# Optimization experiments

Hardware: AMD Instinct MI355X
Metric: run time of the kernel (lower is better)

Reference implementation:

```python
import jax, jax.numpy as jnp
import numpy as np

RS, RC = 3.0, 6.0
N_AXIS = 8
N_NODES, N_ENV, N_EDGES = 50000, 1000000, 200000
N_ATOM = 4
NEURONS = [32, 64, 64]


def setup_inputs() -> dict:
    key = jax.random.key(0)
    ks = jax.random.split(key, 10)
    env_vectors = jax.random.normal(ks[0], (N_ENV, 3), dtype=jnp.float32) * 2.0
    atom_attr = jax.random.uniform(ks[1], (N_NODES, N_ATOM), dtype=jnp.float32)
    env_index = jax.random.randint(ks[2], (2, N_ENV), 0, N_NODES)
    edge_index = jax.random.randint(ks[3], (2, N_EDGES), 0, N_NODES)
    d_in = 2 * N_ATOM + 1  # snorm + both endpoint one-hot attrs
    W1 = jax.random.normal(ks[4], (d_in, NEURONS[0]), dtype=jnp.float32) / np.sqrt(d_in)
    b1 = jnp.zeros((NEURONS[0],), jnp.float32)
    W2 = jax.random.normal(ks[5], (NEURONS[0], NEURONS[1]), dtype=jnp.float32) / np.sqrt(NEURONS[0])
    b2 = jnp.zeros((NEURONS[1],), jnp.float32)
    W3 = jax.random.normal(ks[6], (NEURONS[1], NEURONS[2]), dtype=jnp.float32) / np.sqrt(NEURONS[1])
    b3 = jnp.zeros((NEURONS[2],), jnp.float32)
    return dict(env_vectors=env_vectors, atom_attr=atom_attr, env_index=env_index,
                edge_index=edge_index, W1=W1, b1=b1, W2=W2, b2=b2, W3=W3, b3=b3)


def _smooth(r):
    # elementwise smooth cutoff: 1/r for r<rs, polynomial taper on [rs,rc), 0 beyond
    x = (r - RC) / (RS - RC)
    mid = (1.0 / r) * (x ** 3 * (10.0 + x * (-15.0 + 6.0 * x)) + 1.0)
    return jnp.where(r < RS, 1.0 / r, jnp.where(r < RC, mid, jnp.zeros_like(r)))


def reference(env_vectors, atom_attr, env_index, edge_index, W1, b1, W2, b2, W3, b3):
    n_env = env_vectors.shape[0]
    n_nodes = atom_attr.shape[0]
    r = jnp.linalg.norm(env_vectors, axis=-1, keepdims=True)          # [E,1]
    snorm = _smooth(r)
    # gather both endpoint attrs: env_index.T.flatten() interleaves (src_i, dst_i)
    env_attr = atom_attr[env_index.T.reshape(-1)].reshape(n_env, -1)  # [E, 2*n_atom]
    # ResNet embedding (residual where dims match)
    h = jnp.tanh(jnp.concatenate([snorm, env_attr], axis=-1) @ W1 + b1)
    h = jnp.tanh(h @ W2 + b2)
    h = jnp.tanh(h @ W3 + b3) + h                                     # [E, D]
    # outer product with direction vectors, scatter-mean over target node
    outer = h[:, :, None] * env_vectors[:, None, :]                   # [E, D, 3]
    idx = env_index[1]
    summ = jax.ops.segment_sum(outer, idx, num_segments=n_nodes)      # [N, D, 3]
    cnt = jax.ops.segment_sum(jnp.ones((n_env,), h.dtype), idx, num_segments=n_nodes)
    aggr = summ / jnp.clip(cnt, 1.0)[:, None, None]
    # per-node self outer-product bmm, slice first n_axis columns, flatten
    desc = jnp.einsum('nda,nea->nde', aggr, aggr)[:, :, :N_AXIS]      # [N, D, n_axis]
    node_desc = desc.reshape(n_nodes, -1)                             # [N, D*n_axis]
    edge_desc = node_desc[edge_index[0]] + node_desc[edge_index[1]]   # [Ne, D*n_axis]
    return node_desc, edge_desc
```

## Files before the change

### kernel.cpp

```cpp
#include <hip/hip_runtime.h>
#include <hip/hip_bf16.h>

#define N_NODES 50000
#define N_ENV   1000000
#define N_EDGES 200000

__device__ __forceinline__ float fast_tanh(float x){
  float xc = fminf(fmaxf(x, -10.f), 10.f);
  float t  = __expf(2.f * xc);
  return __fdividef(t - 1.f, t + 1.f);
}

__global__ void k_zero_i(int* __restrict__ p, int n){
  int i = blockIdx.x * blockDim.x + threadIdx.x;
  int stride = gridDim.x * blockDim.x;
  for (; i < n; i += stride) p[i] = 0;
}

__global__ __launch_bounds__(256) void k_hist(
    const int* __restrict__ env_index, int* __restrict__ counts)
{
  int e = blockIdx.x * 256 + threadIdx.x;
  if (e >= N_ENV) return;
  atomicAdd(counts + env_index[N_ENV + e], 1);
}

__global__ __launch_bounds__(64) void k_scan(
    const int* __restrict__ counts, int* __restrict__ offsets,
    int* __restrict__ cursor, float* __restrict__ cnt)
{
  int lane = threadIdx.x;
  int carry = 0;
  for (int base = 0; base < N_NODES; base += 512){
    int i0 = base + lane * 8;
    int c[8];
    #pragma unroll
    for (int j = 0; j < 8; j++){ int i = i0 + j; c[j] = (i < N_NODES) ? counts[i] : 0; }
    int local = 0;
    #pragma unroll
    for (int j = 0; j < 8; j++) local += c[j];
    int incl = local;
    #pragma unroll
    for (int off = 1; off < 64; off <<= 1){
      int t = __shfl_up(incl, off);
      if (lane >= off) incl += t;
    }
    int run = carry + incl - local;
    #pragma unroll
    for (int j = 0; j < 8; j++){
      int i = i0 + j;
      if (i < N_NODES){ offsets[i] = run; cursor[i] = run; cnt[i] = (float)c[j]; }
      run += c[j];
    }
    carry += __shfl(incl, 63);
  }
}

__global__ __launch_bounds__(256) void k_scatter(
    const int* __restrict__ env_index, int* __restrict__ cursor,
    int* __restrict__ order)
{
  int e = blockIdx.x * 256 + threadIdx.x;
  if (e >= N_ENV) return;
  int dst = env_index[N_ENV + e];
  int pos = atomicAdd(cursor + dst, 1);
  order[pos] = e;
}

__global__ __launch_bounds__(256) void k_mlp(
    const float* __restrict__ env_vec, const float* __restrict__ atom_attr,
    const int*  __restrict__ env_index,
    const float* __restrict__ W1, const float* __restrict__ B1,
    const float* __restrict__ W2, const float* __restrict__ B2,
    const float* __restrict__ W3, const float* __restrict__ B3,
    float* __restrict__ h_out)
{
  __shared__ float sW1[32*9];
  __shared__ float sW2[64*32];
  __shared__ float sW3[64*64];
  __shared__ float sB1[32], sB2[64], sB3[64];
  for (int k = threadIdx.x; k < 32*9;  k += 256){ int j = k/9,  i = k%9;  sW1[k] = W1[i*32+j]; }
  for (int k = threadIdx.x; k < 64*32; k += 256){ int j = k>>5, i = k&31; sW2[k] = W2[i*64+j]; }
  for (int k = threadIdx.x; k < 64*64; k += 256){ int j = k>>6, i = k&63; sW3[k] = W3[i*64+j]; }
  if (threadIdx.x < 32) sB1[threadIdx.x] = B1[threadIdx.x];
  if (threadIdx.x < 64) sB2[threadIdx.x] = B2[threadIdx.x];
  if (threadIdx.x < 64) sB3[threadIdx.x] = B3[threadIdx.x];
  __syncthreads();

  int e = blockIdx.x * 256 + threadIdx.x;
  if (e >= N_ENV) return;

  float v0 = env_vec[3*e+0];
  float v1 = env_vec[3*e+1];
  float v2 = env_vec[3*e+2];
  float r = sqrtf(v0*v0 + v1*v1 + v2*v2);
  float invr = 1.f / r;
  float xx = (r - 6.f) * (-1.f/3.f);
  float mid = invr * (xx*xx*xx*(10.f + xx*(-15.f + 6.f*xx)) + 1.f);
  float snorm = (r < 3.f) ? invr : ((r < 6.f) ? mid : 0.f);

  int src = env_index[e];
  int dst = env_index[N_ENV + e];
  (void)dst;

  float x[9];
  x[0] = snorm;
  float4 sa = *reinterpret_cast<const float4*>(atom_attr + src*4);
  float4 da = *reinterpret_cast<const float4*>(atom_attr + env_index[N_ENV + e]*4);
  x[1]=sa.x; x[2]=sa.y; x[3]=sa.z; x[4]=sa.w;
  x[5]=da.x; x[6]=da.y; x[7]=da.z; x[8]=da.w;

  float h1[32];
  #pragma unroll
  for (int j = 0; j < 32; j++){
    float acc = sB1[j];
    #pragma unroll
    for (int i = 0; i < 9; i++) acc += x[i] * sW1[j*9 + i];
    h1[j] = fast_tanh(acc);
  }

  float h2[64];
  #pragma unroll
  for (int j = 0; j < 64; j++){
    float acc = sB2[j];
    #pragma unroll
    for (int i = 0; i < 32; i++) acc += h1[i] * sW2[j*32 + i];
    h2[j] = fast_tanh(acc);
  }

  float* hrow = h_out + (size_t)e * 64;
  float4 hv;
  #pragma unroll
  for (int d = 0; d < 64; d++){
    float acc = sB3[d];
    #pragma unroll
    for (int i = 0; i < 64; i++) acc += h2[i] * sW3[d*64 + i];
    float hd = fast_tanh(acc) + h2[d];
    if      ((d & 3) == 0) hv.x = hd;
    else if ((d & 3) == 1) hv.y = hd;
    else if ((d & 3) == 2) hv.z = hd;
    else { hv.w = hd; *reinterpret_cast<float4*>(hrow + (d - 3)) = hv; }
  }
}

__global__ __launch_bounds__(256) void k_aggr(
    const float* __restrict__ h, const float* __restrict__ env_vec,
    const int* __restrict__ offsets, const int* __restrict__ counts,
    const int* __restrict__ order, float* __restrict__ sums)
{
  int n = blockIdx.x * 256 + threadIdx.x;
  if (n >= N_NODES) return;
  int off = offsets[n];
  int c   = counts[n];
  float acc[192];
  #pragma unroll
  for (int i = 0; i < 192; i++) acc[i] = 0.f;
  for (int k = 0; k < c; k++){
    int e = order[off + k];
    float v0 = env_vec[3*e+0], v1 = env_vec[3*e+1], v2 = env_vec[3*e+2];
    const float4* hr = reinterpret_cast<const float4*>(h + (size_t)e * 64);
    #pragma unroll
    for (int q = 0; q < 16; q++){
      float4 h4 = hr[q];
      const int b = q * 12;
      acc[b+0]  += h4.x * v0; acc[b+1]  += h4.x * v1; acc[b+2]  += h4.x * v2;
      acc[b+3]  += h4.y * v0; acc[b+4]  += h4.y * v1; acc[b+5]  += h4.y * v2;
      acc[b+6]  += h4.z * v0; acc[b+7]  += h4.z * v1; acc[b+8]  += h4.z * v2;
      acc[b+9]  += h4.w * v0; acc[b+10] += h4.w * v1; acc[b+11] += h4.w * v2;
    }
  }
  float* srow = sums + (size_t)n * 192;
  #pragma unroll
  for (int i = 0; i < 192; i += 4)
    *reinterpret_cast<float4*>(srow + i) = make_float4(acc[i], acc[i+1], acc[i+2], acc[i+3]);
}

__global__ __launch_bounds__(256) void k_node(
    const float* __restrict__ sums, const float* __restrict__ cnt,
    float* __restrict__ node_out)
{
  int t = threadIdx.x;
  int node = blockIdx.x * 4 + (t >> 6);
  int d = t & 63;
  const float* srow = sums + (size_t)node * 192;
  float inv = 1.f / fmaxf(cnt[node], 1.f);
  float ad0 = srow[d*3+0] * inv;
  float ad1 = srow[d*3+1] * inv;
  float ad2 = srow[d*3+2] * inv;
  float o[8];
  #pragma unroll
  for (int e2 = 0; e2 < 8; e2++){
    float ae0 = srow[e2*3+0] * inv;
    float ae1 = srow[e2*3+1] * inv;
    float ae2 = srow[e2*3+2] * inv;
    o[e2] = ad0*ae0 + ad1*ae1 + ad2*ae2;
  }
  float* dst = node_out + (size_t)node * 512 + d * 8;
  *reinterpret_cast<float4*>(dst)     = make_float4(o[0], o[1], o[2], o[3]);
  *reinterpret_cast<float4*>(dst + 4) = make_float4(o[4], o[5], o[6], o[7]);
}

__global__ __launch_bounds__(256) void k_edge(
    const float* __restrict__ node_out, const int* __restrict__ edge_index,
    float* __restrict__ edge_out)
{
  int t = threadIdx.x;
  int e = blockIdx.x * 2 + (t >> 7);
  int l = t & 127;
  int s  = edge_index[e];
  int dn = edge_index[N_EDGES + e];
  const float4* rs = reinterpret_cast<const float4*>(node_out + (size_t)s  * 512);
  const float4* rd = reinterpret_cast<const float4*>(node_out + (size_t)dn * 512);
  float4 a = rs[l];
  float4 b = rd[l];
  float4 o = make_float4(a.x + b.x, a.y + b.y, a.z + b.z, a.w + b.w);
  reinterpret_cast<float4*>(edge_out + (size_t)e * 512)[l] = o;
}

extern "C" void kernel_launch(void* const* d_in, const int* in_sizes, int n_in,
                              void* d_out, int out_size, void* d_ws, size_t ws_size,
                              hipStream_t stream) {
  const float* env_vec    = (const float*)d_in[0];
  const float* atom_attr  = (const float*)d_in[1];
  const int*   env_index  = (const int*)  d_in[2];
  const int*   edge_index = (const int*)  d_in[3];
  const float* W1 = (const float*)d_in[4];
  const float* B1 = (const float*)d_in[5];
  const float* W2 = (const float*)d_in[6];
  const float* B2 = (const float*)d_in[7];
  const float* W3 = (const float*)d_in[8];
  const float* B3 = (const float*)d_in[9];

  float* out      = (float*)d_out;
  float* node_out = out;
  float* edge_out = out + (size_t)N_NODES * 512;

  float* scratch = edge_out;
  float* h       = scratch;
  float* sums    = scratch + 64000000;
  float* cnt     = scratch + 73600000;
  int*   counts  = (int*)(scratch + 73700000);
  int*   offsets = (int*)(scratch + 73800000);
  int*   cursor  = (int*)(scratch + 73900000);
  int*   order   = (int*)(scratch + 74000000);

  k_zero_i<<<196, 256, 0, stream>>>(counts, N_NODES);

  k_hist<<<(N_ENV + 255) / 256, 256, 0, stream>>>(env_index, counts);

  k_scan<<<1, 64, 0, stream>>>(counts, offsets, cursor, cnt);

  k_scatter<<<(N_ENV + 255) / 256, 256, 0, stream>>>(env_index, cursor, order);

  k_mlp<<<(N_ENV + 255) / 256, 256, 0, stream>>>(
      env_vec, atom_attr, env_index, W1, B1, W2, B2, W3, B3, h);

  k_aggr<<<(N_NODES + 255) / 256, 256, 0, stream>>>(
      h, env_vec, offsets, counts, order, sums);

  k_node<<<N_NODES / 4, 256, 0, stream>>>(sums, cnt, node_out);

  k_edge<<<N_EDGES / 2, 256, 0, stream>>>(node_out, edge_index, edge_out);
}
```

Before: 1.446 ms.

## Fuse aggregation and node outer product into wave-per-node kernel

```diff
diff --git a/kernel.cpp b/kernel.cpp
--- a/kernel.cpp
+++ b/kernel.cpp
@@ -27,7 +27,7 @@
 
 __global__ __launch_bounds__(64) void k_scan(
     const int* __restrict__ counts, int* __restrict__ offsets,
-    int* __restrict__ cursor, float* __restrict__ cnt)
+    int* __restrict__ cursor)
 {
   int lane = threadIdx.x;
   int carry = 0;
@@ -49,7 +49,7 @@
     #pragma unroll
     for (int j = 0; j < 8; j++){
       int i = i0 + j;
-      if (i < N_NODES){ offsets[i] = run; cursor[i] = run; cnt[i] = (float)c[j]; }
+      if (i < N_NODES){ offsets[i] = run; cursor[i] = run; }
       run += c[j];
     }
     carry += __shfl(incl, 63);
@@ -101,12 +101,11 @@
 
   int src = env_index[e];
   int dst = env_index[N_ENV + e];
-  (void)dst;
 
   float x[9];
   x[0] = snorm;
   float4 sa = *reinterpret_cast<const float4*>(atom_attr + src*4);
-  float4 da = *reinterpret_cast<const float4*>(atom_attr + env_index[N_ENV + e]*4);
+  float4 da = *reinterpret_cast<const float4*>(atom_attr + dst*4);
   x[1]=sa.x; x[2]=sa.y; x[3]=sa.z; x[4]=sa.w;
   x[5]=da.x; x[6]=da.y; x[7]=da.z; x[8]=da.w;
 
@@ -129,73 +128,61 @@
   }
 
   float* hrow = h_out + (size_t)e * 64;
-  float4 hv;
-  #pragma unroll
-  for (int d = 0; d < 64; d++){
-    float acc = sB3[d];
-    #pragma unroll
-    for (int i = 0; i < 64; i++) acc += h2[i] * sW3[d*64 + i];
-    float hd = fast_tanh(acc) + h2[d];
-    if      ((d & 3) == 0) hv.x = hd;
-    else if ((d & 3) == 1) hv.y = hd;
-    else if ((d & 3) == 2) hv.z = hd;
-    else { hv.w = hd; *reinterpret_cast<float4*>(hrow + (d - 3)) = hv; }
-  }
-}
-
-__global__ __launch_bounds__(256) void k_aggr(
+  #pragma unroll
+  for (int dc = 0; dc < 2; dc++){
+    float o[32];
+    #pragma unroll
+    for (int dd = 0; dd < 32; dd++){
+      int d = dc*32 + dd;
+      float acc = sB3[d];
+      #pragma unroll
+      for (int i = 0; i < 64; i++) acc += h2[i] * sW3[d*64 + i];
+      o[dd] = fast_tanh(acc) + h2[d];
+    }
+    #pragma unroll
+    for (int q = 0; q < 8; q++)
+      *reinterpret_cast<float4*>(hrow + dc*32 + q*4) =
+          make_float4(o[q*4], o[q*4+1], o[q*4+2], o[q*4+3]);
+  }
+}
+
+__global__ __launch_bounds__(256) void k_aggr_node(
     const float* __restrict__ h, const float* __restrict__ env_vec,
     const int* __restrict__ offsets, const int* __restrict__ counts,
-    const int* __restrict__ order, float* __restrict__ sums)
-{
-  int n = blockIdx.x * 256 + threadIdx.x;
-  if (n >= N_NODES) return;
-  int off = offsets[n];
-  int c   = counts[n];
-  float acc[192];
-  #pragma unroll
-  for (int i = 0; i < 192; i++) acc[i] = 0.f;
+    const int* __restrict__ order, float* __restrict__ node_out)
+{
+  int wid  = (blockIdx.x * 256 + threadIdx.x) >> 6;
+  int lane = threadIdx.x & 63;
+  if (wid >= N_NODES) return;
+  int off = offsets[wid];
+  int c   = counts[wid];
+
+  float a0 = 0.f, a1 = 0.f, a2 = 0.f;
+  int e = (c > 0) ? order[off] : 0;
   for (int k = 0; k < c; k++){
-    int e = order[off + k];
-    float v0 = env_vec[3*e+0], v1 = env_vec[3*e+1], v2 = env_vec[3*e+2];
-    const float4* hr = reinterpret_cast<const float4*>(h + (size_t)e * 64);
-    #pragma unroll
-    for (int q = 0; q < 16; q++){
-      float4 h4 = hr[q];
-      const int b = q * 12;
-      acc[b+0]  += h4.x * v0; acc[b+1]  += h4.x * v1; acc[b+2]  += h4.x * v2;
-      acc[b+3]  += h4.y * v0; acc[b+4]  += h4.y * v1; acc[b+5]  += h4.y * v2;
-      acc[b+6]  += h4.z * v0; acc[b+7]  += h4.z * v1; acc[b+8]  += h4.z * v2;
-      acc[b+9]  += h4.w * v0; acc[b+10] += h4.w * v1; acc[b+11] += h4.w * v2;
-    }
-  }
-  float* srow = sums + (size_t)n * 192;
-  #pragma unroll
-  for (int i = 0; i < 192; i += 4)
-    *reinterpret_cast<float4*>(srow + i) = make_float4(acc[i], acc[i+1], acc[i+2], acc[i+3]);
-}
-
-__global__ __launch_bounds__(256) void k_node(
-    const float* __restrict__ sums, const float* __restrict__ cnt,
-    float* __restrict__ node_out)
-{
-  int t = threadIdx.x;
-  int node = blockIdx.x * 4 + (t >> 6);
-  int d = t & 63;
-  const float* srow = sums + (size_t)node * 192;
-  float inv = 1.f / fmaxf(cnt[node], 1.f);
-  float ad0 = srow[d*3+0] * inv;
-  float ad1 = srow[d*3+1] * inv;
-  float ad2 = srow[d*3+2] * inv;
+    int eu = __builtin_amdgcn_readfirstlane(e);
+    int en = (k + 1 < c) ? order[off + k + 1] : eu;
+    float hv = h[(size_t)eu * 64 + lane];
+    float v0 = env_vec[3*eu+0];
+    float v1 = env_vec[3*eu+1];
+    float v2 = env_vec[3*eu+2];
+    a0 += hv * v0;
+    a1 += hv * v1;
+    a2 += hv * v2;
+    e = en;
+  }
+  float inv = 1.f / fmaxf((float)c, 1.f);
+  a0 *= inv; a1 *= inv; a2 *= inv;
+
   float o[8];
   #pragma unroll
   for (int e2 = 0; e2 < 8; e2++){
-    float ae0 = srow[e2*3+0] * inv;
-    float ae1 = srow[e2*3+1] * inv;
-    float ae2 = srow[e2*3+2] * inv;
-    o[e2] = ad0*ae0 + ad1*ae1 + ad2*ae2;
-  }
-  float* dst = node_out + (size_t)node * 512 + d * 8;
+    float b0 = __shfl(a0, e2);
+    float b1 = __shfl(a1, e2);
+    float b2 = __shfl(a2, e2);
+    o[e2] = a0*b0 + a1*b1 + a2*b2;
+  }
+  float* dst = node_out + (size_t)wid * 512 + lane * 8;
   *reinterpret_cast<float4*>(dst)     = make_float4(o[0], o[1], o[2], o[3]);
   *reinterpret_cast<float4*>(dst + 4) = make_float4(o[4], o[5], o[6], o[7]);
 }
@@ -237,28 +224,24 @@
 
   float* scratch = edge_out;
   float* h       = scratch;
-  float* sums    = scratch + 64000000;
-  float* cnt     = scratch + 73600000;
-  int*   counts  = (int*)(scratch + 73700000);
-  int*   offsets = (int*)(scratch + 73800000);
-  int*   cursor  = (int*)(scratch + 73900000);
-  int*   order   = (int*)(scratch + 74000000);
+  int*   counts  = (int*)(scratch + 64000000);
+  int*   offsets = (int*)(scratch + 64100000);
+  int*   cursor  = (int*)(scratch + 64200000);
+  int*   order   = (int*)(scratch + 64300000);
 
   k_zero_i<<<196, 256, 0, stream>>>(counts, N_NODES);
 
   k_hist<<<(N_ENV + 255) / 256, 256, 0, stream>>>(env_index, counts);
 
-  k_scan<<<1, 64, 0, stream>>>(counts, offsets, cursor, cnt);
+  k_scan<<<1, 64, 0, stream>>>(counts, offsets, cursor);
 
   k_scatter<<<(N_ENV + 255) / 256, 256, 0, stream>>>(env_index, cursor, order);
 
   k_mlp<<<(N_ENV + 255) / 256, 256, 0, stream>>>(
       env_vec, atom_attr, env_index, W1, B1, W2, B2, W3, B3, h);
 
-  k_aggr<<<(N_NODES + 255) / 256, 256, 0, stream>>>(
-      h, env_vec, offsets, counts, order, sums);
-
-  k_node<<<N_NODES / 4, 256, 0, stream>>>(sums, cnt, node_out);
+  k_aggr_node<<<(N_NODES + 3) / 4, 256, 0, stream>>>(
+      h, env_vec, offsets, counts, order, node_out);
 
   k_edge<<<N_EDGES / 2, 256, 0, stream>>>(node_out, edge_index, edge_out);
 }
```

Result: slower. 1.958 ms (+35.4%).
